# Kernel tuning notes

Measured on AMD Instinct MI355X. Metric: run time of the kernel, lower is better.

The kernel has to match this reference:

```python
import jax, jax.numpy as jnp
import numpy as np

B, T, D, KQ, K, V, L = 4, 4096, 256, 32, 4, 8, 4
LN_EPS = 1e-5


def _layernorm(h, g, b):
    mu = h.mean(-1, keepdims=True)
    var = ((h - mu) ** 2).mean(-1, keepdims=True)
    return (h - mu) * jax.lax.rsqrt(var + LN_EPS) * g + b


def _forward(x, attention_mask, Wq, bq, Wk, bk, Wg, bg, W1f, b1f, W2f, b2f,
             ln_g, ln_b, Whh, b_ih, b_hh, Wp, bp, opW1, opb1, opW2, opb2, Wo, bo):
    # ---- DemandRouter ----
    q = x @ Wq + bq                      # [B,T,KQ]
    k = x @ Wk + bk                      # [B,T,KQ]
    sim = jnp.einsum('btk,bsk->bts', q, k) / jnp.sqrt(jnp.float32(KQ))  # [B,T,T]
    mask2 = attention_mask[:, None, :] * attention_mask[:, :, None]
    sim = jnp.where(mask2 == 0, jnp.float32(-1e9), sim)
    gates = jax.nn.sigmoid(x @ Wg + bg)[..., 0]   # [B,T]
    sim = sim * gates[:, :, None]
    _, idx = jax.lax.top_k(sim, K)                # [B,T,K]
    gathered = jax.vmap(lambda xb, ib: xb[ib])(x, idx)  # [B,T,K,D]
    routed_mean = gathered.mean(axis=2)           # [B,T,D]
    # ---- System1Block ----
    ffn = jax.nn.gelu(routed_mean @ W1f + b1f, approximate=False) @ W2f + b2f
    h = _layernorm(routed_mean + ffn, ln_g, ln_b)  # [B,T,D]
    # ---- ProgramGenerator (GRU over zero inputs, h0 = mean-pooled context) ----
    hs = h.mean(axis=1)                           # [B,D]
    outs = []
    for _ in range(L):
        gh = hs @ Whh.T + b_hh                    # [B,3D]
        r = jax.nn.sigmoid(b_ih[:D] + gh[:, :D])
        z = jax.nn.sigmoid(b_ih[D:2 * D] + gh[:, D:2 * D])
        n = jnp.tanh(b_ih[2 * D:] + r * gh[:, 2 * D:])
        hs = (1 - z) * n + z * hs
        outs.append(hs)
    rnn_out = jnp.stack(outs, axis=1)             # [B,L,D]
    program_logits = rnn_out @ Wp + bp            # [B,L,V]
    # ---- NeuralOpLibrary: op outputs are identical across L, so compute once
    # on [B,T,D] and average softmax weights over L (same math as expand+mean).
    op_hidden = jax.nn.relu(jnp.einsum('btd,vde->btve', h, opW1) + opb1)
    op_out = jnp.einsum('btve,ved->btvd', op_hidden, opW2) + opb2  # [B,T,V,D]
    w = jax.nn.softmax(program_logits, axis=-1).mean(axis=1)       # [B,V]
    fused = jnp.einsum('bv,btvd->btd', w, op_out)                   # [B,T,D]
    # ---- pool + output projection ----
    pooled = fused.max(axis=1)                    # [B,D]
    return pooled @ Wo + bo


def setup_inputs() -> dict:
    key = jax.random.key(0)
    ks = jax.random.split(key, 20)
    s = 0.02
    p = lambda i, shape: jax.random.normal(ks[i], shape, jnp.float32) * s
    return {
        'x': jax.random.normal(ks[0], (B, T, D), jnp.float32),
        'attention_mask': jnp.ones((B, T), jnp.float32),
        'Wq': p(1, (D, KQ)), 'bq': jnp.zeros((KQ,), jnp.float32),
        'Wk': p(2, (D, KQ)), 'bk': jnp.zeros((KQ,), jnp.float32),
        'Wg': p(3, (D, 1)), 'bg': jnp.zeros((1,), jnp.float32),
        'W1f': p(4, (D, 2 * D)), 'b1f': jnp.zeros((2 * D,), jnp.float32),
        'W2f': p(5, (2 * D, D)), 'b2f': jnp.zeros((D,), jnp.float32),
        'ln_g': jnp.ones((D,), jnp.float32), 'ln_b': jnp.zeros((D,), jnp.float32),
        'Whh': p(6, (3 * D, D)), 'b_ih': p(7, (3 * D,)), 'b_hh': p(8, (3 * D,)),
        'Wp': p(9, (D, V)), 'bp': jnp.zeros((V,), jnp.float32),
        'opW1': p(10, (V, D, D)), 'opb1': jnp.zeros((V, D), jnp.float32),
        'opW2': p(11, (V, D, D)), 'opb2': jnp.zeros((V, D), jnp.float32),
        'Wo': p(12, (D, D)), 'bo': jnp.zeros((D,), jnp.float32),
    }


def reference(x, attention_mask, Wq, bq, Wk, bk, Wg, bg, W1f, b1f, W2f, b2f,
              ln_g, ln_b, Whh, b_ih, b_hh, Wp, bp, opW1, opb1, opW2, opb2, Wo, bo):
    return _forward(x, attention_mask, Wq, bq, Wk, bk, Wg, bg, W1f, b1f, W2f, b2f,
                    ln_g, ln_b, Whh, b_ih, b_hh, Wp, bp, opW1, opb1, opW2, opb2, Wo, bo)
```

## Files before the change

### kernel.cpp

```cpp
#include <hip/hip_runtime.h>

#define BB 4
#define TT 4096
#define DD 256
#define KQ 32
#define TOPK 4
#define NV 8
#define NL 4
#define MROWS (BB*TT)
#define NSC 8
#define SSPAN 512
#define NCAND (NSC*16)

typedef __attribute__((ext_vector_type(8))) __bf16 bf16x8;
typedef __attribute__((ext_vector_type(4))) float  f32x4;

__device__ __forceinline__ unsigned short f2bf(float f) {
  union { float f; unsigned u; } un; un.f = f;
  unsigned r = un.u + 0x7fffu + ((un.u >> 16) & 1u);
  return (unsigned short)(r >> 16);
}
__device__ __forceinline__ float b2f(unsigned short s) {
  union { unsigned u; float f; } un; un.u = ((unsigned)s) << 16;
  return un.f;
}
__device__ __forceinline__ void gload16(const unsigned short* g, unsigned short* l) {
  __builtin_amdgcn_global_load_lds((const __attribute__((address_space(1))) void*)(g),
                                   (__attribute__((address_space(3))) void*)(l), 16, 0, 0);
}

__device__ __forceinline__ void ins4(float val, int s, float v[4], int id[4]) {
  if (val <= v[3]) return;
  v[3] = val; id[3] = s;
  #pragma unroll
  for (int j = 3; j > 0; --j) {
    if (v[j] > v[j-1]) {
      float tv = v[j]; v[j] = v[j-1]; v[j-1] = tv;
      int   ti = id[j]; id[j] = id[j-1]; id[j-1] = ti;
    }
  }
}

__global__ __launch_bounds__(256) void prep_weights(
    const float* __restrict__ W1f, const float* __restrict__ W2f,
    const float* __restrict__ opW1, const float* __restrict__ opW2,
    const float* __restrict__ Whh,
    unsigned short* __restrict__ W1ft, unsigned short* __restrict__ W2ft,
    unsigned short* __restrict__ opW1t, unsigned short* __restrict__ opW2t,
    unsigned int* __restrict__ Whhp) {
  int idx = blockIdx.x * 256 + threadIdx.x;
  if (idx < 131072) { int n = idx >> 8, d = idx & 255; W1ft[idx] = f2bf(W1f[d*512 + n]); return; }
  idx -= 131072;
  if (idx < 131072) { int n = idx >> 9, d = idx & 511; W2ft[idx] = f2bf(W2f[d*256 + n]); return; }
  idx -= 131072;
  if (idx < 524288) { int np = idx >> 8, d = idx & 255; int v = np >> 8, e = np & 255;
                      opW1t[idx] = f2bf(opW1[v*65536 + d*256 + e]); return; }
  idx -= 524288;
  if (idx < 524288) { int n = idx >> 11, kp = idx & 2047; int v = kp >> 8, k2 = kp & 255;
                      opW2t[idx] = f2bf(opW2[v*65536 + k2*256 + n]); return; }
  idx -= 524288;
  if (idx < 98304) {
    int dp = idx / 768, j = idx - dp*768;
    unsigned lo = f2bf(Whh[j*256 + 2*dp]);
    unsigned hi = f2bf(Whh[j*256 + 2*dp + 1]);
    Whhp[idx] = lo | (hi << 16);
  }
}

__global__ __launch_bounds__(256) void qk_proj(
    const float* __restrict__ x, const float* __restrict__ Wq, const float* __restrict__ bq,
    const float* __restrict__ Wk, const float* __restrict__ bk,
    float* __restrict__ q, float* __restrict__ kk,
    unsigned short* __restrict__ qbf, unsigned short* __restrict__ kbf) {
  __shared__ float xs[1024];
  int tid = threadIdx.x;
  *(float4*)&xs[tid*4] = *(const float4*)&x[(size_t)blockIdx.x*1024 + tid*4];
  __syncthreads();
  int row = blockIdx.x*4 + (tid >> 6);
  int j = tid & 63;
  int jj = j & 31;
  const float* W = (j < 32) ? Wq : Wk;
  const float* xr = &xs[(tid >> 6) * 256];
  float acc = 0.f;
  #pragma unroll 8
  for (int d = 0; d < 256; ++d) acc += xr[d] * W[d*32 + jj];
  acc += (j < 32) ? bq[jj] : bk[jj];
  float* out = (j < 32) ? q : kk;
  unsigned short* outb = (j < 32) ? qbf : kbf;
  out[(size_t)row*32 + jj] = acc;
  outb[(size_t)row*32 + jj] = f2bf(acc);
}

__global__ __launch_bounds__(256) void sim_scan(
    const unsigned short* __restrict__ qbf, const unsigned short* __restrict__ kbf,
    const float* __restrict__ mask, int* __restrict__ candi, float* __restrict__ candvv) {
  int b = blockIdx.z, sc = blockIdx.y;
  int q0 = blockIdx.x * 64;
  int tid = threadIdx.x;
  int w = tid >> 6, lane = tid & 63;
  int l15 = lane & 15, lhi = lane >> 4;

  __shared__ unsigned short kfr[SSPAN*32];
  __shared__ float ms[SSPAN];
  __shared__ int mflag;

  int qrow = q0 + w*16 + l15;
  bf16x8 qf = *(const bf16x8*)&qbf[((size_t)b*TT + qrow)*32 + lhi*8];
  float mrow = mask[b*TT + qrow];

  float vtop[4]; int itop[4];
  #pragma unroll
  for (int r = 0; r < 4; ++r) { vtop[r] = -__builtin_inff(); itop[r] = 0; }

  int s0 = sc * SSPAN;
  if (tid == 0) mflag = 0;
  __syncthreads();
  int anyzero = 0;
  #pragma unroll
  for (int rr = 0; rr < 2; ++rr) {
    int s = rr*256 + tid;
    const unsigned short* src = &kbf[((size_t)b*TT + s0 + s)*32];
    uint4 d0 = *(const uint4*)(src);
    uint4 d1 = *(const uint4*)(src + 8);
    uint4 d2 = *(const uint4*)(src + 16);
    uint4 d3 = *(const uint4*)(src + 24);
    int fb = (s >> 4)*512 + (s & 15)*8;
    *(uint4*)&kfr[fb +   0] = d0;
    *(uint4*)&kfr[fb + 128] = d1;
    *(uint4*)&kfr[fb + 256] = d2;
    *(uint4*)&kfr[fb + 384] = d3;
    float mv = mask[b*TT + s0 + s];
    ms[s] = mv;
    if (mv == 0.f) anyzero = 1;
  }
  if (anyzero) mflag = 1;
  __syncthreads();
  bool useMask = (mflag != 0) || (mrow == 0.f);
  f32x4 z = {0.f, 0.f, 0.f, 0.f};
  for (int sf = 0; sf < SSPAN/16; sf += 2) {
    bf16x8 a0 = *(const bf16x8*)&kfr[(sf+0)*512 + lane*8];
    bf16x8 a1 = *(const bf16x8*)&kfr[(sf+1)*512 + lane*8];
    f32x4 c0 = __builtin_amdgcn_mfma_f32_16x16x32_bf16(a0, qf, z, 0, 0, 0);
    f32x4 c1 = __builtin_amdgcn_mfma_f32_16x16x32_bf16(a1, qf, z, 0, 0, 0);
    int sb0 = s0 + (sf+0)*16 + lhi*4;
    int sb1 = s0 + (sf+1)*16 + lhi*4;
    #pragma unroll
    for (int r = 0; r < 4; ++r) {
      float v0 = c0[r], v1 = c1[r];
      if (useMask) {
        if (mrow * ms[(sf+0)*16 + lhi*4 + r] == 0.f) v0 = -1e9f;
        if (mrow * ms[(sf+1)*16 + lhi*4 + r] == 0.f) v1 = -1e9f;
      }
      ins4(v0, sb0 + r, vtop, itop);
      ins4(v1, sb1 + r, vtop, itop);
    }
  }
  size_t base = ((size_t)(b*TT + qrow))*NCAND + sc*16 + lhi*4;
  #pragma unroll
  for (int r = 0; r < 4; ++r) { candi[base + r] = itop[r]; candvv[base + r] = vtop[r]; }
}

__global__ __launch_bounds__(256) void refine8(
    const int* __restrict__ candi, const float* __restrict__ candv,
    const float* __restrict__ q, const float* __restrict__ kk,
    const float* __restrict__ mask, int* __restrict__ sel) {
  int tid = threadIdx.x;
  int g = tid >> 5, j = tid & 31;
  int row = blockIdx.x*8 + g;
  int b = row >> 12;
  float v[4]; int id[4];
  const float* cvp = &candv[(size_t)row*NCAND];
  const int*   cip = &candi[(size_t)row*NCAND];
  #pragma unroll
  for (int k2 = 0; k2 < 4; ++k2) { v[k2] = cvp[j + k2*32]; id[k2] = cip[j + k2*32]; }
  int c8[8];
  #pragma unroll
  for (int r = 0; r < 8; ++r) {
    float bv = v[0]; int bi = id[0];
    #pragma unroll
    for (int k2 = 1; k2 < 4; ++k2)
      if (v[k2] > bv || (v[k2] == bv && id[k2] < bi)) { bv = v[k2]; bi = id[k2]; }
    #pragma unroll
    for (int o = 16; o > 0; o >>= 1) {
      float ov = __shfl_xor(bv, o, 32);
      int   oi = __shfl_xor(bi, o, 32);
      if (ov > bv || (ov == bv && oi < bi)) { bv = ov; bi = oi; }
    }
    c8[r] = bi;
    #pragma unroll
    for (int k2 = 0; k2 < 4; ++k2) if (id[k2] == bi) v[k2] = -__builtin_inff();
  }
  int ca = c8[j >> 2];
  int seg = (j & 3) * 8;
  const float* kp = &kk[((size_t)(b << 12) + ca)*32 + seg];
  const float* qp = &q[(size_t)row*32 + seg];
  float pd = 0.f;
  #pragma unroll
  for (int t = 0; t < 8; t += 4) {
    float4 kv = *(const float4*)&kp[t];
    float4 qv = *(const float4*)&qp[t];
    pd += kv.x*qv.x + kv.y*qv.y + kv.z*qv.z + kv.w*qv.w;
  }
  pd += __shfl_xor(pd, 1, 32);
  pd += __shfl_xor(pd, 2, 32);
  if (mask[row] * mask[(b << 12) + ca] == 0.f) pd = -1e9f;
  float dv[8];
  #pragma unroll
  for (int c = 0; c < 8; ++c) dv[c] = __shfl(pd, c*4, 32);
  if (j == 0) {
    int s0 = -1, s1 = -1, s2 = -1, s3 = -1;
    int4 o4;
    #pragma unroll
    for (int r = 0; r < 4; ++r) {
      float bv = -__builtin_inff(); int bi = 0x7fffffff;
      #pragma unroll
      for (int c = 0; c < 8; ++c) {
        int ii = c8[c]; float vv = dv[c];
        if (ii == s0 || ii == s1 || ii == s2 || ii == s3) continue;
        if (vv > bv || (vv == bv && ii < bi)) { bv = vv; bi = ii; }
      }
      if (r == 0) { o4.x = bi; s0 = bi; }
      else if (r == 1) { o4.y = bi; s1 = bi; }
      else if (r == 2) { o4.z = bi; s2 = bi; }
      else { o4.w = bi; s3 = bi; }
    }
    *(int4*)&sel[(size_t)row*4] = o4;
  }
}

__global__ __launch_bounds__(256) void gather_mean(
    const int* __restrict__ sel, const float* __restrict__ x,
    unsigned short* __restrict__ rmb) {
  int tid = threadIdx.x;
  int row = blockIdx.x*4 + (tid >> 6);
  int lane = tid & 63;
  int b = row >> 12;
  int4 s = *(const int4*)&sel[(size_t)row*4];
  const float* xb = &x[(size_t)b*TT*DD];
  float4 a  = *(const float4*)&xb[(size_t)s.x*DD + lane*4];
  float4 bb = *(const float4*)&xb[(size_t)s.y*DD + lane*4];
  float4 cc = *(const float4*)&xb[(size_t)s.z*DD + lane*4];
  float4 e  = *(const float4*)&xb[(size_t)s.w*DD + lane*4];
  ushort4 o;
  o.x = f2bf((a.x + bb.x + cc.x + e.x)*0.25f);
  o.y = f2bf((a.y + bb.y + cc.y + e.y)*0.25f);
  o.z = f2bf((a.z + bb.z + cc.z + e.z)*0.25f);
  o.w = f2bf((a.w + bb.w + cc.w + e.w)*0.25f);
  *(ushort4*)&rmb[(size_t)row*DD + lane*4] = o;
}

__global__ __launch_bounds__(1024) void ffn_fused(
    const unsigned short* __restrict__ rmb,
    const unsigned short* __restrict__ W1ft,
    const unsigned short* __restrict__ W2ft,
    const float* __restrict__ b1f, const float* __restrict__ bias2,
    const float* __restrict__ ln_g, const float* __restrict__ ln_b,
    unsigned short* __restrict__ h) {
  __shared__ unsigned short rmbS[32*264];
  __shared__ unsigned short G1S[32*520];
  __shared__ float psum[32][16];
  __shared__ float psq[32][16];
  __shared__ float meanS[32];
  __shared__ float rstdS[32];
  int tid = threadIdx.x;
  int w = tid >> 6, lane = tid & 63, l16 = lane & 15, lhi = lane >> 4;
  int m0 = blockIdx.x * 32;
  {
    int r = tid >> 5, c = (tid & 31) * 8;
    *(uint4*)&rmbS[r*264 + c] = *(const uint4*)&rmb[(size_t)(m0 + r)*256 + c];
  }
  __syncthreads();
  {
    f32x4 acc1[2][2] = {};
    #pragma unroll
    for (int kk2 = 0; kk2 < 8; ++kk2) {
      int ko = kk2*32 + lhi*8;
      bf16x8 af[2], bf[2];
      af[0] = *(const bf16x8*)&rmbS[l16*264 + ko];
      af[1] = *(const bf16x8*)&rmbS[(16 + l16)*264 + ko];
      bf[0] = *(const bf16x8*)&W1ft[(size_t)(w*32 + l16)*256 + ko];
      bf[1] = *(const bf16x8*)&W1ft[(size_t)(w*32 + 16 + l16)*256 + ko];
      #pragma unroll
      for (int mf = 0; mf < 2; ++mf)
        #pragma unroll
        for (int nf = 0; nf < 2; ++nf)
          acc1[mf][nf] = __builtin_amdgcn_mfma_f32_16x16x32_bf16(af[mf], bf[nf], acc1[mf][nf], 0, 0, 0);
    }
    #pragma unroll
    for (int mf = 0; mf < 2; ++mf) {
      #pragma unroll
      for (int nf = 0; nf < 2; ++nf) {
        int col = w*32 + nf*16 + l16;
        float bias = b1f[col];
        #pragma unroll
        for (int r = 0; r < 4; ++r) {
          int row = mf*16 + lhi*4 + r;
          float v = acc1[mf][nf][r] + bias;
          v = 0.5f * v * (1.0f + erff(v * 0.70710678118654752f));
          G1S[row*520 + col] = f2bf(v);
        }
      }
    }
  }
  __syncthreads();
  f32x4 acc2[2] = {};
  #pragma unroll
  for (int kk2 = 0; kk2 < 16; ++kk2) {
    int ko = kk2*32 + lhi*8;
    bf16x8 af[2], bf;
    af[0] = *(const bf16x8*)&G1S[l16*520 + ko];
    af[1] = *(const bf16x8*)&G1S[(16 + l16)*520 + ko];
    bf = *(const bf16x8*)&W2ft[(size_t)(w*16 + l16)*512 + ko];
    #pragma unroll
    for (int mf = 0; mf < 2; ++mf)
      acc2[mf] = __builtin_amdgcn_mfma_f32_16x16x32_bf16(af[mf], bf, acc2[mf], 0, 0, 0);
  }
  int colc = w*16 + l16;
  float bias2v = bias2[colc];
  float pre[2][4];
  #pragma unroll
  for (int mf = 0; mf < 2; ++mf) {
    #pragma unroll
    for (int r = 0; r < 4; ++r) {
      int row = mf*16 + lhi*4 + r;
      float v = acc2[mf][r] + bias2v + b2f(rmbS[row*264 + colc]);
      pre[mf][r] = v;
      float s = v, sq = v*v;
      #pragma unroll
      for (int o = 1; o < 16; o <<= 1) { s += __shfl_xor(s, o); sq += __shfl_xor(sq, o); }
      if (l16 == 0) { psum[row][w] = s; psq[row][w] = sq; }
    }
  }
  __syncthreads();
  if (tid < 32) {
    float s = 0.f, sq = 0.f;
    #pragma unroll
    for (int j = 0; j < 16; ++j) { s += psum[tid][j]; sq += psq[tid][j]; }
    float mean = s * (1.0f/256.0f);
    float var = sq * (1.0f/256.0f) - mean*mean;
    meanS[tid] = mean;
    rstdS[tid] = rsqrtf(var + 1e-5f);
  }
  __syncthreads();
  float gv = ln_g[colc], bv = ln_b[colc];
  #pragma unroll
  for (int mf = 0; mf < 2; ++mf) {
    #pragma unroll
    for (int r = 0; r < 4; ++r) {
      int row = mf*16 + lhi*4 + r;
      float v = (pre[mf][r] - meanS[row]) * rstdS[row] * gv + bv;
      h[(size_t)(m0 + row)*256 + colc] = f2bf(v);
    }
  }
}

template<int EPI>
__global__ __launch_bounds__(256) void gemm_bf16(
    const unsigned short* __restrict__ A, const unsigned short* __restrict__ Bt,
    int Ndim, int Kdim,
    const float* __restrict__ bias,
    const unsigned short* __restrict__ resB,
    const float* __restrict__ auxf,
    float* __restrict__ outF, unsigned short* __restrict__ outB) {
  __shared__ unsigned short SMEM[128*132];
  unsigned short* As = SMEM;
  unsigned short* Bs = SMEM + 128*64;
  int tid = threadIdx.x;
  int lane = tid & 63, wid = tid >> 6;
  int wm = wid >> 1, wn = wid & 1;
  int l16 = lane & 15, lhi = lane >> 4;
  int m0 = blockIdx.x * 128, n0 = blockIdx.y * 128;
  f32x4 acc[4][4] = {};
  for (int kt = 0; kt < Kdim; kt += 64) {
    __syncthreads();
    #pragma unroll
    for (int i = 0; i < 4; ++i) {
      int L0 = i*256 + wid*64;
      int L  = L0 + lane;
      int r = L >> 3;
      int csrc = ((lane & 7) ^ (r & 7)) * 8;
      gload16(A  + (size_t)(m0 + r)*Kdim + kt + csrc, &As[L0*8]);
      gload16(Bt + (size_t)(n0 + r)*Kdim + kt + csrc, &Bs[L0*8]);
    }
    __syncthreads();
    #pragma unroll
    for (int ks = 0; ks < 2; ++ks) {
      bf16x8 af[4], bfr[4];
      int kc = ks*4 + lhi;
      #pragma unroll
      for (int f = 0; f < 4; ++f) {
        int ra = wm*64 + f*16 + l16;
        af[f]  = *(const bf16x8*)&As[ra*64 + ((kc ^ (ra & 7)))*8];
        int rb = wn*64 + f*16 + l16;
        bfr[f] = *(const bf16x8*)&Bs[rb*64 + ((kc ^ (rb & 7)))*8];
      }
      #pragma unroll
      for (int mf = 0; mf < 4; ++mf)
        #pragma unroll
        for (int nf = 0; nf < 4; ++nf)
          acc[mf][nf] = __builtin_amdgcn_mfma_f32_16x16x32_bf16(af[mf], bfr[nf], acc[mf][nf], 0, 0, 0);
    }
  }
  if constexpr (EPI == 1) {
    #pragma unroll
    for (int mf = 0; mf < 4; ++mf)
      #pragma unroll
      for (int nf = 0; nf < 4; ++nf)
        #pragma unroll
        for (int r = 0; r < 4; ++r) {
          int row = m0 + wm*64 + mf*16 + lhi*4 + r;
          int col = n0 + wn*64 + nf*16 + l16;
          float v = acc[mf][nf][r] + bias[col] + b2f(resB[(size_t)row*Ndim + col]);
          outF[(size_t)row*Ndim + col] = v;
        }
  } else {
    __syncthreads();
    #pragma unroll
    for (int mf = 0; mf < 4; ++mf) {
      #pragma unroll
      for (int nf = 0; nf < 4; ++nf) {
        #pragma unroll
        for (int r = 0; r < 4; ++r) {
          int lrow = wm*64 + mf*16 + lhi*4 + r;
          int lcol = wn*64 + nf*16 + l16;
          int row = m0 + lrow, col = n0 + lcol;
          float v = acc[mf][nf][r];
          if constexpr (EPI == 0) {
            v += bias[col];
            v = 0.5f * v * (1.0f + erff(v * 0.70710678118654752f));
          } else if constexpr (EPI == 2) {
            v += bias[col];
            v = fmaxf(v, 0.0f) * auxf[(row >> 12)*8 + (col >> 8)];
          } else {
            v += auxf[(row >> 12)*256 + col];
          }
          SMEM[lrow*132 + lcol] = f2bf(v);
        }
      }
    }
    __syncthreads();
    #pragma unroll
    for (int i = 0; i < 8; ++i) {
      int idx = i*256 + tid;
      int lrow = idx >> 4, co = (idx & 15)*8;
      *(uint4*)&outB[(size_t)(m0 + lrow)*Ndim + n0 + co] = *(const uint4*)&SMEM[lrow*132 + co];
    }
  }
}

__global__ __launch_bounds__(256) void gemm64_bf16(
    const unsigned short* __restrict__ A, const unsigned short* __restrict__ Bt,
    int Ndim, int Kdim,
    const float* __restrict__ auxf, unsigned short* __restrict__ outB) {
  __shared__ unsigned short SMEM[64*192 + 64];
  unsigned short* As = SMEM;
  unsigned short* Bs = SMEM + 64*64;
  int tid = threadIdx.x;
  int lane = tid & 63, wn = tid >> 6;
  int l16 = lane & 15, lhi = lane >> 4;
  int m0 = blockIdx.x * 64, n0 = blockIdx.y * 128;
  f32x4 acc[4][2] = {};
  for (int kt = 0; kt < Kdim; kt += 64) {
    __syncthreads();
    #pragma unroll
    for (int i = 0; i < 2; ++i) {
      int L0 = i*256 + wn*64;
      int L  = L0 + lane;
      int r = L >> 3;
      int csrc = ((lane & 7) ^ (r & 7)) * 8;
      gload16(A + (size_t)(m0 + r)*Kdim + kt + csrc, &As[L0*8]);
    }
    #pragma unroll
    for (int i = 0; i < 4; ++i) {
      int L0 = i*256 + wn*64;
      int L  = L0 + lane;
      int r = L >> 3;
      int csrc = ((lane & 7) ^ (r & 7)) * 8;
      gload16(Bt + (size_t)(n0 + r)*Kdim + kt + csrc, &Bs[L0*8]);
    }
    __syncthreads();
    #pragma unroll
    for (int ks = 0; ks < 2; ++ks) {
      bf16x8 af[4], bfr[2];
      int kc = ks*4 + lhi;
      #pragma unroll
      for (int f = 0; f < 4; ++f) {
        int ra = f*16 + l16;
        af[f] = *(const bf16x8*)&As[ra*64 + ((kc ^ (ra & 7)))*8];
      }
      #pragma unroll
      for (int f = 0; f < 2; ++f) {
        int rb = wn*32 + f*16 + l16;
        bfr[f] = *(const bf16x8*)&Bs[rb*64 + ((kc ^ (rb & 7)))*8];
      }
      #pragma unroll
      for (int mf = 0; mf < 4; ++mf)
        #pragma unroll
        for (int nf = 0; nf < 2; ++nf)
          acc[mf][nf] = __builtin_amdgcn_mfma_f32_16x16x32_bf16(af[mf], bfr[nf], acc[mf][nf], 0, 0, 0);
    }
  }
  __syncthreads();
  #pragma unroll
  for (int mf = 0; mf < 4; ++mf) {
    #pragma unroll
    for (int nf = 0; nf < 2; ++nf) {
      #pragma unroll
      for (int r = 0; r < 4; ++r) {
        int lrow = mf*16 + lhi*4 + r;
        int lcol = wn*32 + nf*16 + l16;
        float v = acc[mf][nf][r] + auxf[((m0 + lrow) >> 12)*256 + n0 + lcol];
        SMEM[lrow*132 + lcol] = f2bf(v);
      }
    }
  }
  __syncthreads();
  #pragma unroll
  for (int i = 0; i < 4; ++i) {
    int idx = i*256 + tid;
    int lrow = idx >> 4, co = (idx & 15)*8;
    *(uint4*)&outB[(size_t)(m0 + lrow)*Ndim + n0 + co] = *(const uint4*)&SMEM[lrow*132 + co];
  }
}

__global__ __launch_bounds__(256) void hsum_kernel(const unsigned short* __restrict__ h, float* __restrict__ hpart) {
  int c = blockIdx.x, b = blockIdx.y, d = threadIdx.x;
  const unsigned short* hp = &h[((size_t)(b*TT + c*64))*256 + d];
  float s = 0.f;
  #pragma unroll 8
  for (int i = 0; i < 64; ++i) s += b2f(hp[i*256]);
  hpart[(b*64 + c)*256 + d] = s;
}

__global__ __launch_bounds__(1024) void gru_kernel(
    const float* __restrict__ hpart, const unsigned int* __restrict__ Whhp,
    const float* __restrict__ b_ih, const float* __restrict__ b_hh,
    const float* __restrict__ Wp, const float* __restrict__ bp,
    const float* __restrict__ opb2, float* __restrict__ w, float* __restrict__ wb2) {
  int b = blockIdx.x, tid = threadIdx.x;
  __shared__ float hs[256];
  __shared__ float gsh[768];
  __shared__ float wps[2048];
  __shared__ float lgpart[256];
  __shared__ float lg[8];
  __shared__ float wacc[8];
  if (tid < 256) {
    float s = 0.f;
    #pragma unroll
    for (int c = 0; c < 64; ++c) s += hpart[(b*64 + c)*256 + tid];
    hs[tid] = s * (1.0f/4096.0f);
  }
  wps[tid] = Wp[tid];
  wps[1024 + tid] = Wp[1024 + tid];
  if (tid < 8) wacc[tid] = 0.f;
  __syncthreads();
  for (int l = 0; l < NL; ++l) {
    if (tid < 768) {
      float acc = 0.f;
      #pragma unroll 16
      for (int dp = 0; dp < 128; ++dp) {
        unsigned w2 = Whhp[dp*768 + tid];
        acc += b2f((unsigned short)(w2 & 0xffff))*hs[2*dp]
             + b2f((unsigned short)(w2 >> 16))*hs[2*dp + 1];
      }
      gsh[tid] = acc;
    }
    __syncthreads();
    if (tid < 256) {
      float g0 = gsh[tid]       + b_hh[tid];
      float g1 = gsh[256 + tid] + b_hh[256 + tid];
      float g2 = gsh[512 + tid] + b_hh[512 + tid];
      float r = 1.f / (1.f + expf(-(b_ih[tid] + g0)));
      float z = 1.f / (1.f + expf(-(b_ih[256 + tid] + g1)));
      float n = tanhf(b_ih[512 + tid] + r * g2);
      gsh[tid] = (1.f - z) * n + z * hs[tid];
    }
    __syncthreads();
    if (tid < 256) hs[tid] = gsh[tid];
    __syncthreads();
    if (tid < 256) {
      int dp2 = tid >> 3;
      float acc = 0.f;
      #pragma unroll
      for (int k2 = 0; k2 < 8; ++k2) acc += hs[dp2 + 32*k2] * wps[tid + 256*k2];
      lgpart[tid] = acc;
    }
    __syncthreads();
    if (tid < 8) {
      float acc = bp[tid];
      #pragma unroll
      for (int j = 0; j < 32; ++j) acc += lgpart[j*8 + tid];
      lg[tid] = acc;
    }
    __syncthreads();
    if (tid == 0) {
      float mx = lg[0];
      #pragma unroll
      for (int i = 1; i < 8; ++i) mx = fmaxf(mx, lg[i]);
      float sm = 0.f; float e[8];
      #pragma unroll
      for (int i = 0; i < 8; ++i) { e[i] = expf(lg[i] - mx); sm += e[i]; }
      #pragma unroll
      for (int i = 0; i < 8; ++i) wacc[i] += e[i] / sm;
    }
    __syncthreads();
  }
  if (tid < 8) w[b*8 + tid] = wacc[tid] * 0.25f;
  if (tid < 256) {
    float acc = 0.f;
    #pragma unroll
    for (int v = 0; v < 8; ++v) acc += (wacc[v] * 0.25f) * opb2[v*256 + tid];
    wb2[b*256 + tid] = acc;
  }
}

__global__ __launch_bounds__(256) void maxpool_kernel(const unsigned short* __restrict__ fusedB, float* __restrict__ mpart) {
  int c = blockIdx.x, b = blockIdx.y, d = threadIdx.x;
  const unsigned short* fp = &fusedB[((size_t)(b*TT + c*64))*256 + d];
  float m = -__builtin_inff();
  #pragma unroll 8
  for (int i = 0; i < 64; ++i) m = fmaxf(m, b2f(fp[i*256]));
  mpart[(b*64 + c)*256 + d] = m;
}

__global__ __launch_bounds__(256) void outproj_kernel(
    const float* __restrict__ mpart, const float* __restrict__ Wo,
    const float* __restrict__ bo, float* __restrict__ out) {
  int b = blockIdx.x, tid = threadIdx.x;
  __shared__ float pooled[256];
  float m = -__builtin_inff();
  for (int c = 0; c < 64; ++c) m = fmaxf(m, mpart[(b*64 + c)*256 + tid]);
  pooled[tid] = m;
  __syncthreads();
  float acc = bo[tid];
  for (int d = 0; d < 256; ++d) acc += pooled[d] * Wo[d*256 + tid];
  out[b*256 + tid] = acc;
}

extern "C" void kernel_launch(void* const* d_in, const int* in_sizes, int n_in,
                              void* d_out, int out_size, void* d_ws, size_t ws_size,
                              hipStream_t stream) {
  const float* x     = (const float*)d_in[0];
  const float* amask = (const float*)d_in[1];
  const float* Wq    = (const float*)d_in[2];
  const float* bq    = (const float*)d_in[3];
  const float* Wk    = (const float*)d_in[4];
  const float* bk    = (const float*)d_in[5];
  const float* W1f   = (const float*)d_in[8];
  const float* b1f   = (const float*)d_in[9];
  const float* W2f   = (const float*)d_in[10];
  const float* b2fp  = (const float*)d_in[11];
  const float* ln_g  = (const float*)d_in[12];
  const float* ln_b  = (const float*)d_in[13];
  const float* Whh   = (const float*)d_in[14];
  const float* b_ih  = (const float*)d_in[15];
  const float* b_hh  = (const float*)d_in[16];
  const float* Wp    = (const float*)d_in[17];
  const float* bp    = (const float*)d_in[18];
  const float* opW1  = (const float*)d_in[19];
  const float* opb1  = (const float*)d_in[20];
  const float* opW2  = (const float*)d_in[21];
  const float* opb2  = (const float*)d_in[22];
  const float* Wo    = (const float*)d_in[23];
  const float* bo    = (const float*)d_in[24];
  (void)in_sizes; (void)n_in; (void)out_size; (void)ws_size;

  char* ws = (char*)d_ws;
  float*          q      = (float*)(ws + 0);
  float*          kk     = (float*)(ws + 2097152);
  unsigned short* qbf    = (unsigned short*)(ws + 4194304);
  unsigned short* kbf    = (unsigned short*)(ws + 5242880);
  int*            candi  = (int*)(ws + 6291456);
  float*          candv  = (float*)(ws + 14680064);
  unsigned short* rmb    = (unsigned short*)(ws + 23068672);
  unsigned short* G1all  = (unsigned short*)(ws + 0);
  unsigned short* h      = (unsigned short*)(ws + 67108864);
  unsigned short* W1ft   = (unsigned short*)(ws + 75497472);
  unsigned short* W2ft   = (unsigned short*)(ws + 75759616);
  unsigned short* opW1t  = (unsigned short*)(ws + 76021760);
  unsigned short* opW2t  = (unsigned short*)(ws + 77070336);
  unsigned int*   Whhp   = (unsigned int*)(ws + 78118912);
  float*          hpart  = (float*)(ws + 78512128);
  float*          wv     = (float*)(ws + 78774272);
  float*          wb2    = (float*)(ws + 78778368);
  float*          mpart  = (float*)(ws + 78782464);
  unsigned short* fusedB = (unsigned short*)(ws + 79044608);
  int*            sel    = (int*)(ws + 87433216);

  prep_weights<<<5504, 256, 0, stream>>>(W1f, W2f, opW1, opW2, Whh, W1ft, W2ft, opW1t, opW2t, Whhp);
  qk_proj<<<4096, 256, 0, stream>>>(x, Wq, bq, Wk, bk, q, kk, qbf, kbf);
  sim_scan<<<dim3(TT/64, NSC, BB), 256, 0, stream>>>(qbf, kbf, amask, candi, candv);
  refine8<<<MROWS/8, 256, 0, stream>>>(candi, candv, q, kk, amask, sel);
  gather_mean<<<MROWS/4, 256, 0, stream>>>(sel, x, rmb);
  ffn_fused<<<MROWS/32, 1024, 0, stream>>>(rmb, W1ft, W2ft, b1f, b2fp, ln_g, ln_b, h);
  hsum_kernel<<<dim3(64, BB), 256, 0, stream>>>(h, hpart);
  gru_kernel<<<4, 1024, 0, stream>>>(hpart, Whhp, b_ih, b_hh, Wp, bp, opb2, wv, wb2);
  gemm_bf16<2><<<dim3(128, 16), 256, 0, stream>>>(h, opW1t, 2048, 256, opb1, nullptr, wv, nullptr, G1all);
  gemm64_bf16<<<dim3(256, 2), 256, 0, stream>>>(G1all, opW2t, 256, 2048, wb2, fusedB);
  maxpool_kernel<<<dim3(64, BB), 256, 0, stream>>>(fusedB, mpart);
  outproj_kernel<<<4, 256, 0, stream>>>(mpart, Wo, bo, (float*)d_out);
}
```

Baseline: 281.5 us.

## Stage FFN weights through double-buffered swizzled LDS with async global loads

```diff
diff --git a/kernel.cpp b/kernel.cpp
--- a/kernel.cpp
+++ b/kernel.cpp
@@ -258,62 +258,91 @@
     unsigned short* __restrict__ h) {
   __shared__ unsigned short rmbS[32*264];
   __shared__ unsigned short G1S[32*520];
+  __shared__ unsigned short WS[2][16384];
   __shared__ float psum[32][16];
   __shared__ float psq[32][16];
   __shared__ float meanS[32];
   __shared__ float rstdS[32];
   int tid = threadIdx.x;
   int w = tid >> 6, lane = tid & 63, l16 = lane & 15, lhi = lane >> 4;
+  int wb = tid & ~63;
   int m0 = blockIdx.x * 32;
-  {
-    int r = tid >> 5, c = (tid & 31) * 8;
-    *(uint4*)&rmbS[r*264 + c] = *(const uint4*)&rmb[(size_t)(m0 + r)*256 + c];
-  }
-  __syncthreads();
-  {
-    f32x4 acc1[2][2] = {};
-    #pragma unroll
-    for (int kk2 = 0; kk2 < 8; ++kk2) {
-      int ko = kk2*32 + lhi*8;
-      bf16x8 af[2], bf[2];
-      af[0] = *(const bf16x8*)&rmbS[l16*264 + ko];
-      af[1] = *(const bf16x8*)&rmbS[(16 + l16)*264 + ko];
-      bf[0] = *(const bf16x8*)&W1ft[(size_t)(w*32 + l16)*256 + ko];
-      bf[1] = *(const bf16x8*)&W1ft[(size_t)(w*32 + 16 + l16)*256 + ko];
-      #pragma unroll
-      for (int mf = 0; mf < 2; ++mf)
-        #pragma unroll
-        for (int nf = 0; nf < 2; ++nf)
-          acc1[mf][nf] = __builtin_amdgcn_mfma_f32_16x16x32_bf16(af[mf], bf[nf], acc1[mf][nf], 0, 0, 0);
-    }
-    #pragma unroll
-    for (int mf = 0; mf < 2; ++mf) {
-      #pragma unroll
-      for (int nf = 0; nf < 2; ++nf) {
-        int col = w*32 + nf*16 + l16;
-        float bias = b1f[col];
-        #pragma unroll
-        for (int r = 0; r < 4; ++r) {
-          int row = mf*16 + lhi*4 + r;
-          float v = acc1[mf][nf][r] + bias;
-          v = 0.5f * v * (1.0f + erff(v * 0.70710678118654752f));
-          G1S[row*520 + col] = f2bf(v);
-        }
-      }
-    }
-  }
+  { int r = tid >> 5, c = (tid & 31) * 8;
+    *(uint4*)&rmbS[r*264 + c] = *(const uint4*)&rmb[(size_t)(m0 + r)*256 + c]; }
+  #pragma unroll
+  for (int i = 0; i < 2; ++i) {
+    int L0 = i*1024 + wb;
+    int g = L0 + lane;
+    int r = g >> 2, s = g & 3;
+    gload16(&W1ft[(size_t)r*256 + ((s ^ (r & 3))*8)], &WS[0][L0*8]);
+  }
+  __syncthreads();
+  f32x4 acc1[2][2] = {};
+  for (int kk2 = 0; kk2 < 8; ++kk2) {
+    int cur = kk2 & 1;
+    if (kk2 < 7) {
+      int ko0 = (kk2 + 1)*32;
+      #pragma unroll
+      for (int i = 0; i < 2; ++i) {
+        int L0 = i*1024 + wb;
+        int g = L0 + lane;
+        int r = g >> 2, s = g & 3;
+        gload16(&W1ft[(size_t)r*256 + ko0 + ((s ^ (r & 3))*8)], &WS[cur ^ 1][L0*8]);
+      }
+    }
+    int ko = kk2*32 + lhi*8;
+    bf16x8 af[2], bf[2];
+    af[0] = *(const bf16x8*)&rmbS[l16*264 + ko];
+    af[1] = *(const bf16x8*)&rmbS[(16 + l16)*264 + ko];
+    int rb0 = w*32 + l16, rb1 = w*32 + 16 + l16;
+    bf[0] = *(const bf16x8*)&WS[cur][rb0*32 + ((lhi ^ (rb0 & 3))*8)];
+    bf[1] = *(const bf16x8*)&WS[cur][rb1*32 + ((lhi ^ (rb1 & 3))*8)];
+    #pragma unroll
+    for (int mf = 0; mf < 2; ++mf)
+      #pragma unroll
+      for (int nf = 0; nf < 2; ++nf)
+        acc1[mf][nf] = __builtin_amdgcn_mfma_f32_16x16x32_bf16(af[mf], bf[nf], acc1[mf][nf], 0, 0, 0);
+    __syncthreads();
+  }
+  #pragma unroll
+  for (int mf = 0; mf < 2; ++mf) {
+    #pragma unroll
+    for (int nf = 0; nf < 2; ++nf) {
+      int col = w*32 + nf*16 + l16;
+      float bias = b1f[col];
+      #pragma unroll
+      for (int r = 0; r < 4; ++r) {
+        int row = mf*16 + lhi*4 + r;
+        float v = acc1[mf][nf][r] + bias;
+        v = 0.5f * v * (1.0f + erff(v * 0.70710678118654752f));
+        G1S[row*520 + col] = f2bf(v);
+      }
+    }
+  }
+  __syncthreads();
+  { int g = tid;
+    int r = g >> 2, s = g & 3;
+    gload16(&W2ft[(size_t)r*512 + ((s ^ (r & 3))*8)], &WS[0][wb*8]); }
   __syncthreads();
   f32x4 acc2[2] = {};
-  #pragma unroll
   for (int kk2 = 0; kk2 < 16; ++kk2) {
+    int cur = kk2 & 1;
+    if (kk2 < 15) {
+      int ko0 = (kk2 + 1)*32;
+      int g = tid;
+      int r = g >> 2, s = g & 3;
+      gload16(&W2ft[(size_t)r*512 + ko0 + ((s ^ (r & 3))*8)], &WS[cur ^ 1][wb*8]);
+    }
     int ko = kk2*32 + lhi*8;
     bf16x8 af[2], bf;
     af[0] = *(const bf16x8*)&G1S[l16*520 + ko];
     af[1] = *(const bf16x8*)&G1S[(16 + l16)*520 + ko];
-    bf = *(const bf16x8*)&W2ft[(size_t)(w*16 + l16)*512 + ko];
+    int rb = w*16 + l16;
+    bf = *(const bf16x8*)&WS[cur][rb*32 + ((lhi ^ (rb & 3))*8)];
     #pragma unroll
     for (int mf = 0; mf < 2; ++mf)
       acc2[mf] = __builtin_amdgcn_mfma_f32_16x16x32_bf16(af[mf], bf, acc2[mf], 0, 0, 0);
+    __syncthreads();
   }
   int colc = w*16 + l16;
   float bias2v = bias2[colc];
```

After: 277.8 us. About the same (-1.3%).
